# Kernel tuning notes

Hardware: AMD Instinct MI355X
Metric: run time of the kernel (lower is better)

The kernel has to match this reference:

```python
import jax, jax.numpy as jnp
import numpy as np

MOMENTUM = 0.99
EPS = 1e-08


def setup_inputs() -> dict:
    key = jax.random.key(0)
    k1, = jax.random.split(key, 1)
    B, F, T = 32, 257, 3000
    mag = jax.random.uniform(k1, (B, F, T), dtype=jnp.float32)  # magnitudes >= 0
    bias = jnp.zeros((1,), dtype=jnp.float32)
    running_mean = jnp.ones((1,), dtype=jnp.float32)
    return {"mag": mag, "bias": bias, "running_mean": running_mean}


def reference(mag, bias, running_mean):
    """Causal per-frame EMA energy normalization (eval-mode sequence path).

    mag: [B, F, T] -> (mag_norm [B, F, T], mag_mean [B, 1, T])
    """
    B, F, T = mag.shape
    frame_means = mag.mean(axis=1)          # [B, T]
    init = jnp.broadcast_to(running_mean, (B,))  # m_0 = running_mean per batch

    def step(carry, fm_t):
        m = MOMENTUM * carry + (1.0 - MOMENTUM) * fm_t  # [B]
        return m, m

    _, means = jax.lax.scan(step, init, frame_means.T)  # means: [T, B]
    mean_with_bias = means.T + bias[0]                  # [B, T]
    mag_norm = mag / (mean_with_bias[:, None, :] + EPS)  # [B, F, T]
    mag_mean = mean_with_bias[:, None, :]               # [B, 1, T]
    return mag_norm, mag_mean
```

## Files before the change

### kernel.cpp

```cpp
#include <hip/hip_runtime.h>


#define B_  32
#define F_  257
#define T_  3000
#define T4  750
#define NCH 16
#define MOM 0.99f
#define OMM 0.01f
#define EPS_ 1e-8f

__global__ __launch_bounds__(256) void k1_rowsum(const float* __restrict__ mag,
                                                 float* __restrict__ part) {
    const int blk = blockIdx.x;
    const int b   = blk >> 4;
    const int c   = blk & (NCH - 1);
    const int f0  = (c * F_) / NCH;
    const int f1  = ((c + 1) * F_) / NCH;
    const int tid = threadIdx.x;
    const float4* magv = reinterpret_cast<const float4*>(mag);

    float4 a0 = make_float4(0.f, 0.f, 0.f, 0.f);
    float4 a1 = a0, a2 = a0;
    const bool has2 = tid < (T4 - 512);

    int base = (b * F_ + f0) * T4;
    for (int f = f0; f < f1; ++f, base += T4) {
        float4 v0 = magv[base + tid];
        float4 v1 = magv[base + tid + 256];
        a0.x += v0.x; a0.y += v0.y; a0.z += v0.z; a0.w += v0.w;
        a1.x += v1.x; a1.y += v1.y; a1.z += v1.z; a1.w += v1.w;
        if (has2) {
            float4 v2 = magv[base + tid + 512];
            a2.x += v2.x; a2.y += v2.y; a2.z += v2.z; a2.w += v2.w;
        }
    }
    float4* pv = reinterpret_cast<float4*>(part);
    pv[blk * T4 + tid]       = a0;
    pv[blk * T4 + tid + 256] = a1;
    if (has2) pv[blk * T4 + tid + 512] = a2;
}

__global__ __launch_bounds__(256) void k2_scan(const float* __restrict__ part,
                                               const float* __restrict__ bias,
                                               const float* __restrict__ rmean,
                                               float* __restrict__ mag_mean,
                                               float* __restrict__ recip) {
    __shared__ float xs[T_];
    __shared__ float sA[256];
    __shared__ float sB[256];
    const int b = blockIdx.x;
    const int tid = threadIdx.x;

    for (int t = tid; t < T_; t += 256) {
        float s = 0.f;
        #pragma unroll
        for (int c = 0; c < NCH; ++c) s += part[(b * NCH + c) * T_ + t];
        xs[t] = s * (1.0f / F_);
    }
    __syncthreads();

    const int CH = 12;
    const int t0 = tid * CH;
    float A = 1.f, Bv = 0.f;
    if (t0 < T_) {
        #pragma unroll
        for (int j = 0; j < CH; ++j) {
            float x = xs[t0 + j];
            Bv = MOM * Bv + OMM * x;
            A *= MOM;
        }
    }
    sA[tid] = A; sB[tid] = Bv;
    __syncthreads();

    for (int off = 1; off < 256; off <<= 1) {
        float cA = sA[tid], cB = sB[tid];
        float pA = 1.f, pB = 0.f;
        if (tid >= off) { pA = sA[tid - off]; pB = sB[tid - off]; }
        __syncthreads();
        if (tid >= off) { sA[tid] = pA * cA; sB[tid] = pB * cA + cB; }
        __syncthreads();
    }

    float pA = 1.f, pB = 0.f;
    if (tid > 0) { pA = sA[tid - 1]; pB = sB[tid - 1]; }
    __syncthreads();

    const float bias0 = bias[0];
    if (t0 < T_) {
        float m = pA * rmean[0] + pB;
        #pragma unroll
        for (int j = 0; j < CH; ++j) {
            float x = xs[t0 + j];
            m = MOM * m + OMM * x;
            xs[t0 + j] = m + bias0;
        }
    }
    __syncthreads();

    for (int t = tid; t < T_; t += 256) {
        float mb = xs[t];
        mag_mean[b * T_ + t] = mb;
        recip[b * T_ + t]    = 1.0f / (mb + EPS_);
    }
}

__global__ __launch_bounds__(256) void k3_norm(const float* __restrict__ mag,
                                               const float* __restrict__ recip,
                                               float* __restrict__ out) {
    const int r   = blockIdx.x;
    const int b   = r / F_;
    const int tid = threadIdx.x;
    const float4* magv = reinterpret_cast<const float4*>(mag);
    const float4* rv   = reinterpret_cast<const float4*>(recip);
    float4* ov         = reinterpret_cast<float4*>(out);
    const int base  = r * T4;
    const int rbase = b * T4;

    float4 v0 = magv[base + tid];
    float4 r0 = rv[rbase + tid];
    float4 v1 = magv[base + tid + 256];
    float4 r1 = rv[rbase + tid + 256];
    float4 o;
    o.x = v0.x * r0.x; o.y = v0.y * r0.y; o.z = v0.z * r0.z; o.w = v0.w * r0.w;
    ov[base + tid] = o;
    o.x = v1.x * r1.x; o.y = v1.y * r1.y; o.z = v1.z * r1.z; o.w = v1.w * r1.w;
    ov[base + tid + 256] = o;
    if (tid < T4 - 512) {
        float4 v2 = magv[base + tid + 512];
        float4 r2 = rv[rbase + tid + 512];
        o.x = v2.x * r2.x; o.y = v2.y * r2.y; o.z = v2.z * r2.z; o.w = v2.w * r2.w;
        ov[base + tid + 512] = o;
    }
}

extern "C" void kernel_launch(void* const* d_in, const int* in_sizes, int n_in,
                              void* d_out, int out_size, void* d_ws, size_t ws_size,
                              hipStream_t stream) {
    const float* mag   = (const float*)d_in[0];
    const float* bias  = (const float*)d_in[1];
    const float* rmean = (const float*)d_in[2];
    float* out      = (float*)d_out;
    float* mag_mean = out + (size_t)B_ * F_ * T_;
    float* part  = (float*)d_ws;
    float* recip = part + (size_t)B_ * NCH * T_;

    k1_rowsum<<<B_ * NCH, 256, 0, stream>>>(mag, part);
    k2_scan<<<B_, 256, 0, stream>>>(part, bias, rmean, mag_mean, recip);
    k3_norm<<<B_ * F_, 256, 0, stream>>>(mag, recip, out);
}
```

Measured before the change: 203.9 us.

## Fuse rowsum, scan and normalize into one cooperative kernel with grid syncs

Replaces the three separate launches (partial row sums, per-batch EMA scan, normalization) with a single cooperative kernel that uses two grid-wide syncs between phases. In the normalize phase each block reuses the same 16-row chunk of mag it summed in the first phase, and it stages the reciprocal means in shared memory. The aim is to cut launch gaps and let the second read of mag hit in cache. The cost is that normalization now runs on only 512 blocks looping over rows instead of one block per row, which lowers memory-level parallelism. While the 32 scan blocks work, every other block idles at the grid barrier.

```diff
diff --git a/kernel.cpp b/kernel.cpp
--- a/kernel.cpp
+++ b/kernel.cpp
@@ -1,4 +1,7 @@
 #include <hip/hip_runtime.h>
+#include <hip/hip_cooperative_groups.h>
+
+namespace cg = cooperative_groups;
 
 
 #define B_  32
@@ -10,128 +13,131 @@
 #define OMM 0.01f
 #define EPS_ 1e-8f
 
-__global__ __launch_bounds__(256) void k1_rowsum(const float* __restrict__ mag,
-                                                 float* __restrict__ part) {
+__global__ __launch_bounds__(256) void ema_fused(const float* __restrict__ mag,
+                                                 const float* __restrict__ bias,
+                                                 const float* __restrict__ rmean,
+                                                 float* __restrict__ out,
+                                                 float* __restrict__ mag_mean,
+                                                 float* __restrict__ part,
+                                                 float* __restrict__ recip) {
+    cg::grid_group grid = cg::this_grid();
+    __shared__ float4 xs4[T4];
+    float* xs = reinterpret_cast<float*>(xs4);
+    __shared__ float sA[256];
+    __shared__ float sB[256];
+
     const int blk = blockIdx.x;
     const int b   = blk >> 4;
     const int c   = blk & (NCH - 1);
-    const int f0  = (c * F_) / NCH;
-    const int f1  = ((c + 1) * F_) / NCH;
+    const int f0  = (c * F_) >> 4;
+    const int f1  = ((c + 1) * F_) >> 4;
     const int tid = threadIdx.x;
     const float4* magv = reinterpret_cast<const float4*>(mag);
 
-    float4 a0 = make_float4(0.f, 0.f, 0.f, 0.f);
-    float4 a1 = a0, a2 = a0;
-    const bool has2 = tid < (T4 - 512);
+    {
+        float4 a0 = make_float4(0.f, 0.f, 0.f, 0.f);
+        float4 a1 = a0, a2 = a0;
+        const bool has2 = tid < (T4 - 512);
+        int base = (b * F_ + f0) * T4;
+        for (int f = f0; f < f1; ++f, base += T4) {
+            float4 v0 = magv[base + tid];
+            float4 v1 = magv[base + tid + 256];
+            a0.x += v0.x; a0.y += v0.y; a0.z += v0.z; a0.w += v0.w;
+            a1.x += v1.x; a1.y += v1.y; a1.z += v1.z; a1.w += v1.w;
+            if (has2) {
+                float4 v2 = magv[base + tid + 512];
+                a2.x += v2.x; a2.y += v2.y; a2.z += v2.z; a2.w += v2.w;
+            }
+        }
+        float4* pv = reinterpret_cast<float4*>(part);
+        pv[blk * T4 + tid]       = a0;
+        pv[blk * T4 + tid + 256] = a1;
+        if (has2) pv[blk * T4 + tid + 512] = a2;
+    }
 
-    int base = (b * F_ + f0) * T4;
-    for (int f = f0; f < f1; ++f, base += T4) {
-        float4 v0 = magv[base + tid];
-        float4 v1 = magv[base + tid + 256];
-        a0.x += v0.x; a0.y += v0.y; a0.z += v0.z; a0.w += v0.w;
-        a1.x += v1.x; a1.y += v1.y; a1.z += v1.z; a1.w += v1.w;
-        if (has2) {
-            float4 v2 = magv[base + tid + 512];
-            a2.x += v2.x; a2.y += v2.y; a2.z += v2.z; a2.w += v2.w;
+    grid.sync();
+
+    if (blk < B_) {
+        const int bb = blk;
+        for (int t = tid; t < T_; t += 256) {
+            float s = 0.f;
+            #pragma unroll
+            for (int cc = 0; cc < NCH; ++cc) s += part[(bb * NCH + cc) * T_ + t];
+            xs[t] = s * (1.0f / F_);
+        }
+        __syncthreads();
+
+        const int CH = 12;
+        const int t0 = tid * CH;
+        float A = 1.f, Bv = 0.f;
+        if (t0 < T_) {
+            #pragma unroll
+            for (int j = 0; j < CH; ++j) {
+                Bv = MOM * Bv + OMM * xs[t0 + j];
+                A *= MOM;
+            }
+        }
+        sA[tid] = A; sB[tid] = Bv;
+        __syncthreads();
+
+        for (int off = 1; off < 256; off <<= 1) {
+            float cA = sA[tid], cB = sB[tid];
+            float pA = 1.f, pB = 0.f;
+            if (tid >= off) { pA = sA[tid - off]; pB = sB[tid - off]; }
+            __syncthreads();
+            if (tid >= off) { sA[tid] = pA * cA; sB[tid] = pB * cA + cB; }
+            __syncthreads();
+        }
+
+        float pA = 1.f, pB = 0.f;
+        if (tid > 0) { pA = sA[tid - 1]; pB = sB[tid - 1]; }
+        __syncthreads();
+
+        const float bias0 = bias[0];
+        if (t0 < T_) {
+            float m = pA * rmean[0] + pB;
+            #pragma unroll
+            for (int j = 0; j < CH; ++j) {
+                m = MOM * m + OMM * xs[t0 + j];
+                xs[t0 + j] = m + bias0;
+            }
+        }
+        __syncthreads();
+
+        for (int t = tid; t < T_; t += 256) {
+            float mb = xs[t];
+            mag_mean[bb * T_ + t] = mb;
+            recip[bb * T_ + t]    = 1.0f / (mb + EPS_);
         }
     }
-    float4* pv = reinterpret_cast<float4*>(part);
-    pv[blk * T4 + tid]       = a0;
-    pv[blk * T4 + tid + 256] = a1;
-    if (has2) pv[blk * T4 + tid + 512] = a2;
-}
 
-__global__ __launch_bounds__(256) void k2_scan(const float* __restrict__ part,
-                                               const float* __restrict__ bias,
-                                               const float* __restrict__ rmean,
-                                               float* __restrict__ mag_mean,
-                                               float* __restrict__ recip) {
-    __shared__ float xs[T_];
-    __shared__ float sA[256];
-    __shared__ float sB[256];
-    const int b = blockIdx.x;
-    const int tid = threadIdx.x;
+    grid.sync();
 
-    for (int t = tid; t < T_; t += 256) {
-        float s = 0.f;
-        #pragma unroll
-        for (int c = 0; c < NCH; ++c) s += part[(b * NCH + c) * T_ + t];
-        xs[t] = s * (1.0f / F_);
-    }
-    __syncthreads();
+    {
+        const float4* rv = reinterpret_cast<const float4*>(recip);
+        for (int i = tid; i < T4; i += 256) xs4[i] = rv[b * T4 + i];
+        __syncthreads();
 
-    const int CH = 12;
-    const int t0 = tid * CH;
-    float A = 1.f, Bv = 0.f;
-    if (t0 < T_) {
-        #pragma unroll
-        for (int j = 0; j < CH; ++j) {
-            float x = xs[t0 + j];
-            Bv = MOM * Bv + OMM * x;
-            A *= MOM;
+        float4* ov = reinterpret_cast<float4*>(out);
+        int base = (b * F_ + f0) * T4;
+        const bool has2 = tid < (T4 - 512);
+        const float4 r0 = xs4[tid];
+        const float4 r1 = xs4[tid + 256];
+        const float4 r2 = has2 ? xs4[tid + 512] : r0;
+        for (int f = f0; f < f1; ++f, base += T4) {
+            float4 v0 = magv[base + tid];
+            float4 v1 = magv[base + tid + 256];
+            float4 o;
+            o.x = v0.x * r0.x; o.y = v0.y * r0.y; o.z = v0.z * r0.z; o.w = v0.w * r0.w;
+            ov[base + tid] = o;
+            o.x = v1.x * r1.x; o.y = v1.y * r1.y; o.z = v1.z * r1.z; o.w = v1.w * r1.w;
+            ov[base + tid + 256] = o;
+            if (has2) {
+                float4 v2 = magv[base + tid + 512];
+                o.x = v2.x * r2.x; o.y = v2.y * r2.y; o.z = v2.z * r2.z; o.w = v2.w * r2.w;
+                ov[base + tid + 512] = o;
+            }
         }
-    }
-    sA[tid] = A; sB[tid] = Bv;
-    __syncthreads();
-
-    for (int off = 1; off < 256; off <<= 1) {
-        float cA = sA[tid], cB = sB[tid];
-        float pA = 1.f, pB = 0.f;
-        if (tid >= off) { pA = sA[tid - off]; pB = sB[tid - off]; }
-        __syncthreads();
-        if (tid >= off) { sA[tid] = pA * cA; sB[tid] = pB * cA + cB; }
-        __syncthreads();
-    }
-
-    float pA = 1.f, pB = 0.f;
-    if (tid > 0) { pA = sA[tid - 1]; pB = sB[tid - 1]; }
-    __syncthreads();
-
-    const float bias0 = bias[0];
-    if (t0 < T_) {
-        float m = pA * rmean[0] + pB;
-        #pragma unroll
-        for (int j = 0; j < CH; ++j) {
-            float x = xs[t0 + j];
-            m = MOM * m + OMM * x;
-            xs[t0 + j] = m + bias0;
-        }
-    }
-    __syncthreads();
-
-    for (int t = tid; t < T_; t += 256) {
-        float mb = xs[t];
-        mag_mean[b * T_ + t] = mb;
-        recip[b * T_ + t]    = 1.0f / (mb + EPS_);
-    }
-}
-
-__global__ __launch_bounds__(256) void k3_norm(const float* __restrict__ mag,
-                                               const float* __restrict__ recip,
-                                               float* __restrict__ out) {
-    const int r   = blockIdx.x;
-    const int b   = r / F_;
-    const int tid = threadIdx.x;
-    const float4* magv = reinterpret_cast<const float4*>(mag);
-    const float4* rv   = reinterpret_cast<const float4*>(recip);
-    float4* ov         = reinterpret_cast<float4*>(out);
-    const int base  = r * T4;
-    const int rbase = b * T4;
-
-    float4 v0 = magv[base + tid];
-    float4 r0 = rv[rbase + tid];
-    float4 v1 = magv[base + tid + 256];
-    float4 r1 = rv[rbase + tid + 256];
-    float4 o;
-    o.x = v0.x * r0.x; o.y = v0.y * r0.y; o.z = v0.z * r0.z; o.w = v0.w * r0.w;
-    ov[base + tid] = o;
-    o.x = v1.x * r1.x; o.y = v1.y * r1.y; o.z = v1.z * r1.z; o.w = v1.w * r1.w;
-    ov[base + tid + 256] = o;
-    if (tid < T4 - 512) {
-        float4 v2 = magv[base + tid + 512];
-        float4 r2 = rv[rbase + tid + 512];
-        o.x = v2.x * r2.x; o.y = v2.y * r2.y; o.z = v2.z * r2.z; o.w = v2.w * r2.w;
-        ov[base + tid + 512] = o;
     }
 }
 
@@ -146,7 +152,8 @@
     float* part  = (float*)d_ws;
     float* recip = part + (size_t)B_ * NCH * T_;
 
-    k1_rowsum<<<B_ * NCH, 256, 0, stream>>>(mag, part);
-    k2_scan<<<B_, 256, 0, stream>>>(part, bias, rmean, mag_mean, recip);
-    k3_norm<<<B_ * F_, 256, 0, stream>>>(mag, recip, out);
+    void* args[] = {(void*)&mag, (void*)&bias, (void*)&rmean,
+                    (void*)&out, (void*)&mag_mean, (void*)&part, (void*)&recip};
+    hipLaunchCooperativeKernel((const void*)ema_fused, dim3(B_ * NCH), dim3(256),
+                               args, 0, stream);
 }
```

Result: slower. 320.4 us (+57.2%).
